# Kernel tuning notes

Measured on AMD Instinct MI355X. Metric: run time of the kernel, lower is better.

## Reference

```python
import jax, jax.numpy as jnp
import numpy as np

B, S, H = 4, 2048, 768
NUM_HEADS = 12
HEAD_DIM = H // NUM_HEADS


def setup_inputs() -> dict:
    key = jax.random.key(0)
    k1, k2, k3 = jax.random.split(key, 3)
    hidden_states = jax.random.normal(k1, (B, S, H), dtype=jnp.float32)
    # torch Linear weight [out,in]; store transposed [in,out] for x @ W
    w_qkv = jax.random.normal(k2, (H, 3 * H), dtype=jnp.float32) * (1.0 / np.sqrt(H))
    w_out = jax.random.normal(k3, (H, H), dtype=jnp.float32) * (1.0 / np.sqrt(H))
    return {"hidden_states": hidden_states, "w_qkv": w_qkv, "w_out": w_out}


def reference(hidden_states, w_qkv, w_out):
    b, s, h = hidden_states.shape
    qkv = hidden_states @ w_qkv                      # [b,s,3h]
    qkv = qkv.reshape(b, s, 3, NUM_HEADS, HEAD_DIM)
    qkv = jnp.transpose(qkv, (2, 0, 3, 1, 4))        # [3,b,nh,s,hd]
    q, k, v = qkv[0], qkv[1], qkv[2]
    scale = 1.0 / np.sqrt(HEAD_DIM).astype(np.float32)
    scores = jnp.einsum('bhqd,bhkd->bhqk', q, k) * scale   # [b,nh,s,s]
    causal = jnp.triu(jnp.ones((s, s), dtype=bool), k=1)
    scores = jnp.where(causal, jnp.float32(-jnp.inf), scores)
    attn = jax.nn.softmax(scores, axis=-1)
    # dropout is identity in eval mode
    out = jnp.einsum('bhqk,bhkd->bhqd', attn, v)      # [b,nh,s,hd]
    out = jnp.transpose(out, (0, 2, 1, 3)).reshape(b, s, h)
    return out @ w_out
```

## Files before the change

kernel.cpp:

```cpp
#include <hip/hip_runtime.h>
#include <stdint.h>

#define B_ 4
#define S_ 2048
#define H_ 768
#define NH_ 12
#define HD_ 64
#define BH_ (B_ * NH_)

#define QSCALE 0.18033688011112042f

typedef __attribute__((ext_vector_type(4))) float f32x4;
typedef __attribute__((ext_vector_type(16))) float f32x16;
typedef __attribute__((ext_vector_type(8))) __bf16 bf16x8;
typedef __attribute__((ext_vector_type(8))) unsigned short ushort8;
typedef __attribute__((ext_vector_type(2))) unsigned int u32x2;
typedef __attribute__((ext_vector_type(4))) unsigned int u32x4;

__device__ __forceinline__ unsigned short bf16rne(float f) {
  union { float f; unsigned int u; } v;
  v.f = f;
  unsigned int u = v.u;
  return (unsigned short)((u + 0x7fffu + ((u >> 16) & 1u)) >> 16);
}

#if __has_builtin(__builtin_amdgcn_cvt_pk_bf16_f32)
__device__ __forceinline__ unsigned int pk2(float a, float b) {
  auto r = __builtin_amdgcn_cvt_pk_bf16_f32(a, b);
  return *(unsigned int*)&r;
}
#else
__device__ __forceinline__ unsigned int pk2(float a, float b) {
  return (unsigned int)bf16rne(a) | ((unsigned int)bf16rne(b) << 16);
}
#endif

#if __has_builtin(__builtin_amdgcn_exp2f)
#define EXP2F(x) __builtin_amdgcn_exp2f(x)
#else
#define EXP2F(x) exp2f(x)
#endif

#if __has_builtin(__builtin_amdgcn_permlane32_swap)
__device__ __forceinline__ u32x2 permswap(unsigned a, unsigned b) {
  u32x2 r = __builtin_amdgcn_permlane32_swap(a, b, false, false);
  return r;
}
#else
__device__ __forceinline__ u32x2 permswap(unsigned a, unsigned b) {
  int l = (int)(threadIdx.x & 63);
  unsigned ap = (unsigned)__shfl((int)a, l ^ 32, 64);
  unsigned bp = (unsigned)__shfl((int)b, l ^ 32, 64);
  u32x2 r;
  r[0] = (l & 32) ? bp : a;
  r[1] = (l & 32) ? b : ap;
  return r;
}
#endif

__device__ __forceinline__ void gll16(const void* g, void* l) {
  __builtin_amdgcn_global_load_lds(
      (const __attribute__((address_space(1))) unsigned int*)g,
      (__attribute__((address_space(3))) unsigned int*)l, 16, 0, 0);
}

__device__ __forceinline__ void tconv_body(const float* __restrict__ in,
                                           unsigned short* __restrict__ out,
                                           int R, int C, int bx, int by,
                                           unsigned short (*tile)[72], int tid) {
  int c0 = bx * 64, r0 = by * 64;
#pragma unroll
  for (int i = 0; i < 4; ++i) {
    int c = i * 256 + tid;
    int row = c >> 4, col4 = (c & 15) * 4;
    float4 v = *(const float4*)(in + (size_t)(r0 + row) * C + c0 + col4);
    *(uint2*)(&tile[row][col4]) = (uint2){pk2(v.x, v.y), pk2(v.z, v.w)};
  }
  __syncthreads();
#pragma unroll
  for (int i = 0; i < 2; ++i) {
    int c = i * 256 + tid;
    int oc = c >> 3, r8 = (c & 7) * 8;
    ushort8 v;
#pragma unroll
    for (int j = 0; j < 8; ++j) v[j] = tile[r8 + j][oc];
    *(ushort8*)(out + (size_t)(c0 + oc) * R + r0 + r8) = v;
  }
}

__global__ __launch_bounds__(256) void prep_kernel(const float* __restrict__ hs,
                                                   const float* __restrict__ wqkv,
                                                   const float* __restrict__ wout,
                                                   unsigned short* __restrict__ Xbf,
                                                   unsigned short* __restrict__ Wqkvt,
                                                   unsigned short* __restrict__ Woutt) {
  __shared__ unsigned short tile[64][72];
  int bid = blockIdx.x, tid = threadIdx.x;
  if (bid < 3072) {
    int i = (bid * 256 + tid) * 8;
    const float4* p = (const float4*)(hs + i);
    float4 a = p[0], b = p[1];
    uint4 r = {pk2(a.x, a.y), pk2(a.z, a.w), pk2(b.x, b.y), pk2(b.z, b.w)};
    *(uint4*)(Xbf + i) = r;
  } else if (bid < 3504) {
    int idx = bid - 3072;
    tconv_body(wqkv, Wqkvt, 768, 2304, idx % 36, idx / 36, tile, tid);
  } else {
    int idx = bid - 3504;
    tconv_body(wout, Woutt, 768, 768, idx % 12, idx / 12, tile, tid);
  }
}

template <int MODE>
__device__ __forceinline__ void gemm_core(const unsigned short* __restrict__ A,
                                          const unsigned short* __restrict__ Bm,
                                          void* __restrict__ Cout, int N, int K,
                                          int bm, int bn,
                                          unsigned short* As, unsigned short* Bs) {
  int tid = threadIdx.x;
  int lane = tid & 63, wave = tid >> 6;
  int quad = lane >> 4, l16 = lane & 15;
  int wm = (wave & 1) * 64, wn = (wave >> 1) * 64;
  const unsigned short* Ag = A + (size_t)bm * 128 * K;
  const unsigned short* Bg = Bm + (size_t)bn * 128 * K;

  f32x4 zero = {0.f, 0.f, 0.f, 0.f};
  f32x4 acc[4][4];
#pragma unroll
  for (int mt = 0; mt < 4; ++mt)
#pragma unroll
    for (int nt = 0; nt < 4; ++nt) acc[mt][nt] = zero;

  for (int k0 = 0; k0 < K; k0 += 32) {
#pragma unroll
    for (int i = 0; i < 2; ++i) {
      int c = i * 256 + tid;
      int row = c >> 2, off = (c & 3) * 8;
      gll16(Ag + (size_t)row * K + k0 + off, As + c * 8);
      gll16(Bg + (size_t)row * K + k0 + off, Bs + c * 8);
    }
    __syncthreads();
    bf16x8 af[4], bf[4];
#pragma unroll
    for (int mt = 0; mt < 4; ++mt)
      af[mt] = *(const bf16x8*)(As + (wm + mt * 16 + l16) * 32 + quad * 8);
#pragma unroll
    for (int nt = 0; nt < 4; ++nt)
      bf[nt] = *(const bf16x8*)(Bs + (wn + nt * 16 + l16) * 32 + quad * 8);
#pragma unroll
    for (int mt = 0; mt < 4; ++mt)
#pragma unroll
      for (int nt = 0; nt < 4; ++nt) {
        if (MODE == 2)
          acc[mt][nt] = __builtin_amdgcn_mfma_f32_16x16x32_bf16(af[mt], bf[nt], acc[mt][nt], 0, 0, 0);
        else
          acc[mt][nt] = __builtin_amdgcn_mfma_f32_16x16x32_bf16(bf[nt], af[mt], acc[mt][nt], 0, 0, 0);
      }
    __syncthreads();
  }

  if (MODE == 0) {
    unsigned short* qkv = (unsigned short*)Cout;
    int which = (bn >= 6);
#pragma unroll
    for (int mt = 0; mt < 4; ++mt)
#pragma unroll
      for (int nt = 0; nt < 4; ++nt) {
        int f0 = bn * 128 + wn + nt * 16 + quad * 4;
        int tm = bm * 128 + wm + mt * 16 + l16;
        int rem = f0 - which * 768;
        int head = rem >> 6, d0 = rem & 63;
        int b = tm >> 11, s = tm & 2047;
        if (which == 0) {
          uint2 pkv = {pk2(acc[mt][nt][0] * QSCALE, acc[mt][nt][1] * QSCALE),
                       pk2(acc[mt][nt][2] * QSCALE, acc[mt][nt][3] * QSCALE)};
          *(uint2*)(qkv + (((size_t)b * NH_ + head) * S_ + s) * HD_ + d0) = pkv;
        } else {
          uint2 pkv = {pk2(acc[mt][nt][0], acc[mt][nt][1]),
                       pk2(acc[mt][nt][2], acc[mt][nt][3])};
          int t = s >> 6, kb = (s >> 5) & 1, row = s & 31;
          int dk = d0 >> 4, hh = (d0 >> 3) & 1, off = d0 & 7;
          *(uint2*)(qkv + ((size_t)(BH_ + b * NH_ + head)) * S_ * HD_ + t * 4096
                    + ((kb * 4 + dk) * 64 + hh * 32 + row) * 8 + off) = pkv;
        }
      }
  } else if (MODE == 2) {
    unsigned short* vt = (unsigned short*)Cout;
#pragma unroll
    for (int mt = 0; mt < 4; ++mt)
#pragma unroll
      for (int nt = 0; nt < 4; ++nt) {
        int f = bn * 128 + wn + nt * 16 + l16;
        int t0 = bm * 128 + wm + mt * 16 + quad * 4;
        int rem = f - 1536;
        int head = rem >> 6, d = rem & 63;
        int b = t0 >> 11, s0 = t0 & 2047;
        int tile = s0 >> 6, sin = s0 & 63;
        int ks = sin >> 4, hh = (sin >> 3) & 1, off = sin & 7;
        int db = d >> 5, drow = d & 31;
        uint2 pkv = {pk2(acc[mt][nt][0], acc[mt][nt][1]),
                     pk2(acc[mt][nt][2], acc[mt][nt][3])};
        *(uint2*)(vt + ((size_t)(b * NH_ + head)) * HD_ * S_ + tile * 4096
                  + ((db * 4 + ks) * 64 + hh * 32 + drow) * 8 + off) = pkv;
      }
  } else {
    float* outp = (float*)Cout;
#pragma unroll
    for (int mt = 0; mt < 4; ++mt)
#pragma unroll
      for (int nt = 0; nt < 4; ++nt) {
        int f0 = bn * 128 + wn + nt * 16 + quad * 4;
        int tm = bm * 128 + wm + mt * 16 + l16;
        *(f32x4*)(outp + (size_t)tm * N + f0) = acc[mt][nt];
      }
  }
}

__global__ __launch_bounds__(256) void gemm_qkv(const unsigned short* __restrict__ A,
                                                const unsigned short* __restrict__ Bm,
                                                unsigned short* __restrict__ QK,
                                                unsigned short* __restrict__ Vt) {
  __shared__ unsigned short As[128 * 32];
  __shared__ unsigned short Bs[128 * 32];
  int bm = blockIdx.x, bn = blockIdx.y;
  if (bn < 12)
    gemm_core<0>(A, Bm, QK, 2304, 768, bm, bn, As, Bs);
  else
    gemm_core<2>(A, Bm, Vt, 2304, 768, bm, bn, As, Bs);
}

__global__ __launch_bounds__(256) void gemm_out(const unsigned short* __restrict__ A,
                                                const unsigned short* __restrict__ Bm,
                                                float* __restrict__ Cout) {
  __shared__ unsigned short As[128 * 32];
  __shared__ unsigned short Bs[128 * 32];
  gemm_core<1>(A, Bm, Cout, 768, 768, blockIdx.x, blockIdx.y, As, Bs);
}

__global__ __launch_bounds__(256, 4) void attn_kernel(const unsigned short* __restrict__ Q,
                                                      const unsigned short* __restrict__ Kg,
                                                      const unsigned short* __restrict__ Vt,
                                                      unsigned short* __restrict__ O) {
  __shared__ unsigned short Ks[2][64 * 64];
  __shared__ unsigned short Vs[2][64 * 64];
  const int pi_[16] = {0, 1, 3, 5, 7, 9, 11, 13, 15, 14, 12, 10, 8, 6, 4, 2};
  int bh = blockIdx.x;
  int y = blockIdx.y;
  int qt = pi_[(bh + y) & 15];
  int tid = threadIdx.x, lane = tid & 63, wave = tid >> 6;
  int l32 = lane & 31, h = lane >> 5;
  const unsigned short* Qp = Q + (size_t)bh * S_ * HD_;
  int q0 = qt * 128;
  int qrow = q0 + wave * 32 + l32;
  int kmax_w = (q0 + wave * 32 + 31) >> 6;
  int kmax_b = 2 * qt + 1;

  const unsigned short* kS = Kg + (size_t)bh * S_ * HD_;
  const unsigned short* vS = Vt + (size_t)bh * HD_ * S_;

  auto stage = [&](int t, int buf) {
#pragma unroll
    for (int i = 0; i < 2; ++i) {
      int c = (i * 256 + tid) * 8;
      gll16(kS + (size_t)t * 4096 + c, &Ks[buf][c]);
      gll16(vS + (size_t)t * 4096 + c, &Vs[buf][c]);
    }
  };

  stage(0, 0);

  bf16x8 qf[4];
#pragma unroll
  for (int dk = 0; dk < 4; ++dk)
    qf[dk] = *(const bf16x8*)(Qp + (size_t)qrow * HD_ + dk * 16 + h * 8);

  bf16x8 ones;
#pragma unroll
  for (int j = 0; j < 8; ++j) ones[j] = (__bf16)1.0f;

  const int flin = lane * 8;

  f32x16 zero16;
#pragma unroll
  for (int j = 0; j < 16; ++j) zero16[j] = 0.f;
  f32x16 o[2], rsv;
  o[0] = zero16; o[1] = zero16; rsv = zero16;

  auto body = [&](int t, const unsigned short* Kb, const unsigned short* Vb) {
    f32x16 sf[2];
    sf[0] = zero16; sf[1] = zero16;
#pragma unroll
    for (int kb = 0; kb < 2; ++kb)
#pragma unroll
      for (int dk = 0; dk < 4; ++dk) {
        bf16x8 kf = *(const bf16x8*)(Kb + (kb * 4 + dk) * 512 + flin);
        sf[kb] = __builtin_amdgcn_mfma_f32_32x32x16_bf16(kf, qf[dk], sf[kb], 0, 0, 0);
      }

    if (t == kmax_w) {
#pragma unroll
      for (int kb = 0; kb < 2; ++kb)
#pragma unroll
        for (int r = 0; r < 16; ++r)
          if (t * 64 + kb * 32 + (r & 3) + 8 * (r >> 2) + 4 * h > qrow) sf[kb][r] = -1e30f;
    }

    unsigned p01[8], p23[8];
#pragma unroll
    for (int kb = 0; kb < 2; ++kb)
#pragma unroll
      for (int g = 0; g < 4; ++g) {
        p01[kb * 4 + g] = pk2(EXP2F(sf[kb][g * 4 + 0]), EXP2F(sf[kb][g * 4 + 1]));
        p23[kb * 4 + g] = pk2(EXP2F(sf[kb][g * 4 + 2]), EXP2F(sf[kb][g * 4 + 3]));
      }

#pragma unroll
    for (int ks = 0; ks < 4; ++ks) {
      u32x2 a02 = permswap(p01[2 * ks], p01[2 * ks + 1]);
      u32x2 a13 = permswap(p23[2 * ks], p23[2 * ks + 1]);
      u32x4 pu;
      pu[0] = a02[0]; pu[1] = a13[0]; pu[2] = a02[1]; pu[3] = a13[1];
      bf16x8 pf = *(bf16x8*)&pu;
      rsv = __builtin_amdgcn_mfma_f32_32x32x16_bf16(ones, pf, rsv, 0, 0, 0);
#pragma unroll
      for (int db = 0; db < 2; ++db) {
        bf16x8 vf = *(const bf16x8*)(Vb + (db * 4 + ks) * 512 + flin);
        o[db] = __builtin_amdgcn_mfma_f32_32x32x16_bf16(vf, pf, o[db], 0, 0, 0);
      }
    }
  };

  for (int t = 0; t <= kmax_b; t += 2) {
    __syncthreads();
    stage(t + 1, 1);
    if (t <= kmax_w) body(t, &Ks[0][0], &Vs[0][0]);
    __syncthreads();
    if (t + 2 <= kmax_b) stage(t + 2, 0);
    if (t + 1 <= kmax_w) body(t + 1, &Ks[1][0], &Vs[1][0]);
  }

  float inv = 1.f / rsv[0];
  int b = bh / NH_, hh = bh % NH_;
#pragma unroll
  for (int db = 0; db < 2; ++db)
#pragma unroll
    for (int g = 0; g < 4; ++g) {
      uint2 pkv = {pk2(o[db][g * 4 + 0] * inv, o[db][g * 4 + 1] * inv),
                   pk2(o[db][g * 4 + 2] * inv, o[db][g * 4 + 3] * inv)};
      int d0 = db * 32 + 8 * g + 4 * h;
      *(uint2*)(O + ((size_t)b * S_ + qrow) * H_ + hh * HD_ + d0) = pkv;
    }
}

extern "C" void kernel_launch(void* const* d_in, const int* in_sizes, int n_in,
                              void* d_out, int out_size, void* d_ws, size_t ws_size,
                              hipStream_t stream) {
  (void)in_sizes; (void)n_in; (void)out_size; (void)ws_size;
  const float* hs = (const float*)d_in[0];
  const float* wqkv = (const float*)d_in[1];
  const float* wout = (const float*)d_in[2];
  float* out = (float*)d_out;

  unsigned short* Xbf = (unsigned short*)d_ws;
  unsigned short* Wqkvt = Xbf + (size_t)8192 * 768;
  unsigned short* Woutt = Wqkvt + (size_t)2304 * 768;
  unsigned short* QK = Woutt + (size_t)768 * 768;
  unsigned short* Vt = QK + (size_t)2 * BH_ * S_ * HD_;
  unsigned short* Attn = Xbf;

  prep_kernel<<<3648, 256, 0, stream>>>(hs, wqkv, wout, Xbf, Wqkvt, Woutt);
  gemm_qkv<<<dim3(64, 18), 256, 0, stream>>>(Xbf, Wqkvt, QK, Vt);
  attn_kernel<<<dim3(48, 16), 256, 0, stream>>>(QK, QK + (size_t)BH_ * S_ * HD_, Vt, Attn);
  gemm_out<<<dim3(64, 6), 256, 0, stream>>>(Attn, Woutt, out);
}
```

Baseline: 198.2 us.

## Make attention kernel persistent with atomic work queue, longest tiles first

Replaces the static 48x16 attention grid with 1280 persistent blocks that pull (q-tile, head) jobs from a global atomic counter, with the longest causal tiles handed out first. The counter is reset inside the prep kernel. The aim is to balance the triangular causal workload across CUs and shorten the tail. In exchange it adds an atomic and two barriers per job, and it can lose the locality that the old permuted static order gave.

Result: slower. 212.0 us (+6.9%).

```diff
diff --git a/kernel.cpp b/kernel.cpp
--- a/kernel.cpp
+++ b/kernel.cpp
@@ -93,9 +93,11 @@
                                                    const float* __restrict__ wout,
                                                    unsigned short* __restrict__ Xbf,
                                                    unsigned short* __restrict__ Wqkvt,
-                                                   unsigned short* __restrict__ Woutt) {
+                                                   unsigned short* __restrict__ Woutt,
+                                                   unsigned int* __restrict__ ctr) {
   __shared__ unsigned short tile[64][72];
   int bid = blockIdx.x, tid = threadIdx.x;
+  if (bid == 0 && tid == 0) *ctr = 0u;
   if (bid < 3072) {
     int i = (bid * 256 + tid) * 8;
     const float4* p = (const float4*)(hs + i);
@@ -239,117 +241,125 @@
 
 __global__ __launch_bounds__(256, 4) void attn_kernel(const unsigned short* __restrict__ Q,
                                                       const unsigned short* __restrict__ Kg,
-                                                      const unsigned short* __restrict__ Vt,
-                                                      unsigned short* __restrict__ O) {
+                                                      const unsigned short* __restrict__ Vtg,
+                                                      unsigned short* __restrict__ O,
+                                                      unsigned int* __restrict__ ctr) {
   __shared__ unsigned short Ks[2][64 * 64];
   __shared__ unsigned short Vs[2][64 * 64];
-  const int pi_[16] = {0, 1, 3, 5, 7, 9, 11, 13, 15, 14, 12, 10, 8, 6, 4, 2};
-  int bh = blockIdx.x;
-  int y = blockIdx.y;
-  int qt = pi_[(bh + y) & 15];
+  __shared__ unsigned int jobS;
   int tid = threadIdx.x, lane = tid & 63, wave = tid >> 6;
   int l32 = lane & 31, h = lane >> 5;
-  const unsigned short* Qp = Q + (size_t)bh * S_ * HD_;
-  int q0 = qt * 128;
-  int qrow = q0 + wave * 32 + l32;
-  int kmax_w = (q0 + wave * 32 + 31) >> 6;
-  int kmax_b = 2 * qt + 1;
-
-  const unsigned short* kS = Kg + (size_t)bh * S_ * HD_;
-  const unsigned short* vS = Vt + (size_t)bh * HD_ * S_;
-
-  auto stage = [&](int t, int buf) {
-#pragma unroll
-    for (int i = 0; i < 2; ++i) {
-      int c = (i * 256 + tid) * 8;
-      gll16(kS + (size_t)t * 4096 + c, &Ks[buf][c]);
-      gll16(vS + (size_t)t * 4096 + c, &Vs[buf][c]);
+  const int flin = lane * 8;
+
+  bf16x8 ones;
+#pragma unroll
+  for (int j = 0; j < 8; ++j) ones[j] = (__bf16)1.0f;
+
+  f32x16 zero16;
+#pragma unroll
+  for (int j = 0; j < 16; ++j) zero16[j] = 0.f;
+
+  for (;;) {
+    __syncthreads();
+    if (tid == 0) jobS = atomicAdd(ctr, 1u);
+    __syncthreads();
+    unsigned j = jobS;
+    if (j >= 768u) break;
+    int qt = 15 - (int)(j / 48u);
+    int bh = (int)(j % 48u);
+
+    const unsigned short* Qp = Q + (size_t)bh * S_ * HD_;
+    const unsigned short* kS = Kg + (size_t)bh * S_ * HD_;
+    const unsigned short* vS = Vtg + (size_t)bh * HD_ * S_;
+    int q0 = qt * 128;
+    int qrow = q0 + wave * 32 + l32;
+    int kmax_w = (q0 + wave * 32 + 31) >> 6;
+    int kmax_b = 2 * qt + 1;
+
+    auto stage = [&](int t, int buf) {
+#pragma unroll
+      for (int i = 0; i < 2; ++i) {
+        int c = (i * 256 + tid) * 8;
+        gll16(kS + (size_t)t * 4096 + c, &Ks[buf][c]);
+        gll16(vS + (size_t)t * 4096 + c, &Vs[buf][c]);
+      }
+    };
+
+    stage(0, 0);
+
+    bf16x8 qf[4];
+#pragma unroll
+    for (int dk = 0; dk < 4; ++dk)
+      qf[dk] = *(const bf16x8*)(Qp + (size_t)qrow * HD_ + dk * 16 + h * 8);
+
+    f32x16 o[2], rsv;
+    o[0] = zero16; o[1] = zero16; rsv = zero16;
+
+    auto body = [&](int t, const unsigned short* Kb, const unsigned short* Vb) {
+      f32x16 sf[2];
+      sf[0] = zero16; sf[1] = zero16;
+#pragma unroll
+      for (int kb = 0; kb < 2; ++kb)
+#pragma unroll
+        for (int dk = 0; dk < 4; ++dk) {
+          bf16x8 kf = *(const bf16x8*)(Kb + (kb * 4 + dk) * 512 + flin);
+          sf[kb] = __builtin_amdgcn_mfma_f32_32x32x16_bf16(kf, qf[dk], sf[kb], 0, 0, 0);
+        }
+
+      if (t == kmax_w) {
+#pragma unroll
+        for (int kb = 0; kb < 2; ++kb)
+#pragma unroll
+          for (int r = 0; r < 16; ++r)
+            if (t * 64 + kb * 32 + (r & 3) + 8 * (r >> 2) + 4 * h > qrow) sf[kb][r] = -1e30f;
+      }
+
+      unsigned p01[8], p23[8];
+#pragma unroll
+      for (int kb = 0; kb < 2; ++kb)
+#pragma unroll
+        for (int g = 0; g < 4; ++g) {
+          p01[kb * 4 + g] = pk2(EXP2F(sf[kb][g * 4 + 0]), EXP2F(sf[kb][g * 4 + 1]));
+          p23[kb * 4 + g] = pk2(EXP2F(sf[kb][g * 4 + 2]), EXP2F(sf[kb][g * 4 + 3]));
+        }
+
+#pragma unroll
+      for (int ks = 0; ks < 4; ++ks) {
+        u32x2 a02 = permswap(p01[2 * ks], p01[2 * ks + 1]);
+        u32x2 a13 = permswap(p23[2 * ks], p23[2 * ks + 1]);
+        u32x4 pu;
+        pu[0] = a02[0]; pu[1] = a13[0]; pu[2] = a02[1]; pu[3] = a13[1];
+        bf16x8 pf = *(bf16x8*)&pu;
+        rsv = __builtin_amdgcn_mfma_f32_32x32x16_bf16(ones, pf, rsv, 0, 0, 0);
+#pragma unroll
+        for (int db = 0; db < 2; ++db) {
+          bf16x8 vf = *(const bf16x8*)(Vb + (db * 4 + ks) * 512 + flin);
+          o[db] = __builtin_amdgcn_mfma_f32_32x32x16_bf16(vf, pf, o[db], 0, 0, 0);
+        }
+      }
+    };
+
+    for (int t = 0; t <= kmax_b; t += 2) {
+      __syncthreads();
+      stage(t + 1, 1);
+      if (t <= kmax_w) body(t, &Ks[0][0], &Vs[0][0]);
+      __syncthreads();
+      if (t + 2 <= kmax_b) stage(t + 2, 0);
+      if (t + 1 <= kmax_w) body(t + 1, &Ks[1][0], &Vs[1][0]);
     }
-  };
-
-  stage(0, 0);
-
-  bf16x8 qf[4];
-#pragma unroll
-  for (int dk = 0; dk < 4; ++dk)
-    qf[dk] = *(const bf16x8*)(Qp + (size_t)qrow * HD_ + dk * 16 + h * 8);
-
-  bf16x8 ones;
-#pragma unroll
-  for (int j = 0; j < 8; ++j) ones[j] = (__bf16)1.0f;
-
-  const int flin = lane * 8;
-
-  f32x16 zero16;
-#pragma unroll
-  for (int j = 0; j < 16; ++j) zero16[j] = 0.f;
-  f32x16 o[2], rsv;
-  o[0] = zero16; o[1] = zero16; rsv = zero16;
-
-  auto body = [&](int t, const unsigned short* Kb, const unsigned short* Vb) {
-    f32x16 sf[2];
-    sf[0] = zero16; sf[1] = zero16;
-#pragma unroll
-    for (int kb = 0; kb < 2; ++kb)
-#pragma unroll
-      for (int dk = 0; dk < 4; ++dk) {
-        bf16x8 kf = *(const bf16x8*)(Kb + (kb * 4 + dk) * 512 + flin);
-        sf[kb] = __builtin_amdgcn_mfma_f32_32x32x16_bf16(kf, qf[dk], sf[kb], 0, 0, 0);
-      }
-
-    if (t == kmax_w) {
-#pragma unroll
-      for (int kb = 0; kb < 2; ++kb)
-#pragma unroll
-        for (int r = 0; r < 16; ++r)
-          if (t * 64 + kb * 32 + (r & 3) + 8 * (r >> 2) + 4 * h > qrow) sf[kb][r] = -1e30f;
-    }
-
-    unsigned p01[8], p23[8];
-#pragma unroll
-    for (int kb = 0; kb < 2; ++kb)
+
+    float inv = 1.f / rsv[0];
+    int b = bh / NH_, hh = bh % NH_;
+#pragma unroll
+    for (int db = 0; db < 2; ++db)
 #pragma unroll
       for (int g = 0; g < 4; ++g) {
-        p01[kb * 4 + g] = pk2(EXP2F(sf[kb][g * 4 + 0]), EXP2F(sf[kb][g * 4 + 1]));
-        p23[kb * 4 + g] = pk2(EXP2F(sf[kb][g * 4 + 2]), EXP2F(sf[kb][g * 4 + 3]));
-      }
-
-#pragma unroll
-    for (int ks = 0; ks < 4; ++ks) {
-      u32x2 a02 = permswap(p01[2 * ks], p01[2 * ks + 1]);
-      u32x2 a13 = permswap(p23[2 * ks], p23[2 * ks + 1]);
-      u32x4 pu;
-      pu[0] = a02[0]; pu[1] = a13[0]; pu[2] = a02[1]; pu[3] = a13[1];
-      bf16x8 pf = *(bf16x8*)&pu;
-      rsv = __builtin_amdgcn_mfma_f32_32x32x16_bf16(ones, pf, rsv, 0, 0, 0);
-#pragma unroll
-      for (int db = 0; db < 2; ++db) {
-        bf16x8 vf = *(const bf16x8*)(Vb + (db * 4 + ks) * 512 + flin);
-        o[db] = __builtin_amdgcn_mfma_f32_32x32x16_bf16(vf, pf, o[db], 0, 0, 0);
-      }
-    }
-  };
-
-  for (int t = 0; t <= kmax_b; t += 2) {
-    __syncthreads();
-    stage(t + 1, 1);
-    if (t <= kmax_w) body(t, &Ks[0][0], &Vs[0][0]);
-    __syncthreads();
-    if (t + 2 <= kmax_b) stage(t + 2, 0);
-    if (t + 1 <= kmax_w) body(t + 1, &Ks[1][0], &Vs[1][0]);
-  }
-
-  float inv = 1.f / rsv[0];
-  int b = bh / NH_, hh = bh % NH_;
-#pragma unroll
-  for (int db = 0; db < 2; ++db)
-#pragma unroll
-    for (int g = 0; g < 4; ++g) {
-      uint2 pkv = {pk2(o[db][g * 4 + 0] * inv, o[db][g * 4 + 1] * inv),
-                   pk2(o[db][g * 4 + 2] * inv, o[db][g * 4 + 3] * inv)};
-      int d0 = db * 32 + 8 * g + 4 * h;
-      *(uint2*)(O + ((size_t)b * S_ + qrow) * H_ + hh * HD_ + d0) = pkv;
-    }
+        uint2 pkv = {pk2(o[db][g * 4 + 0] * inv, o[db][g * 4 + 1] * inv),
+                     pk2(o[db][g * 4 + 2] * inv, o[db][g * 4 + 3] * inv)};
+        int d0 = db * 32 + 8 * g + 4 * h;
+        *(uint2*)(O + ((size_t)b * S_ + qrow) * H_ + hh * HD_ + d0) = pkv;
+      }
+  }
 }
 
 extern "C" void kernel_launch(void* const* d_in, const int* in_sizes, int n_in,
@@ -366,10 +376,11 @@
   unsigned short* Woutt = Wqkvt + (size_t)2304 * 768;
   unsigned short* QK = Woutt + (size_t)768 * 768;
   unsigned short* Vt = QK + (size_t)2 * BH_ * S_ * HD_;
+  unsigned int* ctr = (unsigned int*)(Vt + (size_t)BH_ * HD_ * S_);
   unsigned short* Attn = Xbf;
 
-  prep_kernel<<<3648, 256, 0, stream>>>(hs, wqkv, wout, Xbf, Wqkvt, Woutt);
+  prep_kernel<<<3648, 256, 0, stream>>>(hs, wqkv, wout, Xbf, Wqkvt, Woutt, ctr);
   gemm_qkv<<<dim3(64, 18), 256, 0, stream>>>(Xbf, Wqkvt, QK, Vt);
-  attn_kernel<<<dim3(48, 16), 256, 0, stream>>>(QK, QK + (size_t)BH_ * S_ * HD_, Vt, Attn);
+  attn_kernel<<<1280, 256, 0, stream>>>(QK, QK + (size_t)BH_ * S_ * HD_, Vt, Attn, ctr);
   gemm_out<<<dim3(64, 6), 256, 0, stream>>>(Attn, Woutt, out);
 }
```

## Use 64-row tiles for output GEMM and add MFMA priority hints in attention

Applied to the files above, without the earlier changes.

Replaces the output-projection GEMM, which used shared 128x128 tiles over 384 blocks, with a dedicated 64x128-tile kernel launched as 768 blocks so the 256 CUs are better filled. The attention kernel also wraps its MFMA sections in s_setprio to raise wave priority during matrix ops, aiming to overlap other waves' exp and softmax work. The new GEMM has no double buffering and lower per-block reuse. The priority hints may have little effect.

New measurement: 195.3 us. About the same (-1.5%).

```diff
diff --git a/kernel.cpp b/kernel.cpp
--- a/kernel.cpp
+++ b/kernel.cpp
@@ -184,7 +184,7 @@
                     + ((kb * 4 + dk) * 64 + hh * 32 + row) * 8 + off) = pkv;
         }
       }
-  } else if (MODE == 2) {
+  } else {
     unsigned short* vt = (unsigned short*)Cout;
 #pragma unroll
     for (int mt = 0; mt < 4; ++mt)
@@ -203,16 +203,6 @@
         *(uint2*)(vt + ((size_t)(b * NH_ + head)) * HD_ * S_ + tile * 4096
                   + ((db * 4 + ks) * 64 + hh * 32 + drow) * 8 + off) = pkv;
       }
-  } else {
-    float* outp = (float*)Cout;
-#pragma unroll
-    for (int mt = 0; mt < 4; ++mt)
-#pragma unroll
-      for (int nt = 0; nt < 4; ++nt) {
-        int f0 = bn * 128 + wn + nt * 16 + quad * 4;
-        int tm = bm * 128 + wm + mt * 16 + l16;
-        *(f32x4*)(outp + (size_t)tm * N + f0) = acc[mt][nt];
-      }
   }
 }
 
@@ -229,12 +219,61 @@
     gemm_core<2>(A, Bm, Vt, 2304, 768, bm, bn, As, Bs);
 }
 
-__global__ __launch_bounds__(256) void gemm_out(const unsigned short* __restrict__ A,
-                                                const unsigned short* __restrict__ Bm,
-                                                float* __restrict__ Cout) {
-  __shared__ unsigned short As[128 * 32];
+__global__ __launch_bounds__(256) void gemm_out64(const unsigned short* __restrict__ A,
+                                                  const unsigned short* __restrict__ Bm,
+                                                  float* __restrict__ Cout) {
+  __shared__ unsigned short As[64 * 32];
   __shared__ unsigned short Bs[128 * 32];
-  gemm_core<1>(A, Bm, Cout, 768, 768, blockIdx.x, blockIdx.y, As, Bs);
+  const int K = 768, N = 768;
+  int bm = blockIdx.x, bn = blockIdx.y;
+  int tid = threadIdx.x, lane = tid & 63, wave = tid >> 6;
+  int quad = lane >> 4, l16 = lane & 15;
+  int wn = wave * 32;
+  const unsigned short* Ag = A + (size_t)bm * 64 * K;
+  const unsigned short* Bg = Bm + (size_t)bn * 128 * K;
+
+  f32x4 zero = {0.f, 0.f, 0.f, 0.f};
+  f32x4 acc[4][2];
+#pragma unroll
+  for (int mt = 0; mt < 4; ++mt)
+#pragma unroll
+    for (int nt = 0; nt < 2; ++nt) acc[mt][nt] = zero;
+
+  for (int k0 = 0; k0 < K; k0 += 32) {
+    {
+      int row = tid >> 2, off = (tid & 3) * 8;
+      gll16(Ag + (size_t)row * K + k0 + off, As + tid * 8);
+    }
+#pragma unroll
+    for (int i = 0; i < 2; ++i) {
+      int c = i * 256 + tid;
+      int row = c >> 2, off = (c & 3) * 8;
+      gll16(Bg + (size_t)row * K + k0 + off, Bs + c * 8);
+    }
+    __syncthreads();
+    bf16x8 af[4], bf[2];
+#pragma unroll
+    for (int mt = 0; mt < 4; ++mt)
+      af[mt] = *(const bf16x8*)(As + (mt * 16 + l16) * 32 + quad * 8);
+#pragma unroll
+    for (int nt = 0; nt < 2; ++nt)
+      bf[nt] = *(const bf16x8*)(Bs + (wn + nt * 16 + l16) * 32 + quad * 8);
+#pragma unroll
+    for (int mt = 0; mt < 4; ++mt)
+#pragma unroll
+      for (int nt = 0; nt < 2; ++nt)
+        acc[mt][nt] = __builtin_amdgcn_mfma_f32_16x16x32_bf16(bf[nt], af[mt], acc[mt][nt], 0, 0, 0);
+    __syncthreads();
+  }
+
+#pragma unroll
+  for (int mt = 0; mt < 4; ++mt)
+#pragma unroll
+    for (int nt = 0; nt < 2; ++nt) {
+      int f0 = bn * 128 + wn + nt * 16 + quad * 4;
+      int tm = bm * 64 + mt * 16 + l16;
+      *(f32x4*)(Cout + (size_t)tm * N + f0) = acc[mt][nt];
+    }
 }
 
 __global__ __launch_bounds__(256, 4) void attn_kernel(const unsigned short* __restrict__ Q,
@@ -289,6 +328,7 @@
   auto body = [&](int t, const unsigned short* Kb, const unsigned short* Vb) {
     f32x16 sf[2];
     sf[0] = zero16; sf[1] = zero16;
+    __builtin_amdgcn_s_setprio(1);
 #pragma unroll
     for (int kb = 0; kb < 2; ++kb)
 #pragma unroll
@@ -296,6 +336,7 @@
         bf16x8 kf = *(const bf16x8*)(Kb + (kb * 4 + dk) * 512 + flin);
         sf[kb] = __builtin_amdgcn_mfma_f32_32x32x16_bf16(kf, qf[dk], sf[kb], 0, 0, 0);
       }
+    __builtin_amdgcn_s_setprio(0);
 
     if (t == kmax_w) {
 #pragma unroll
@@ -321,12 +362,14 @@
       u32x4 pu;
       pu[0] = a02[0]; pu[1] = a13[0]; pu[2] = a02[1]; pu[3] = a13[1];
       bf16x8 pf = *(bf16x8*)&pu;
+      __builtin_amdgcn_s_setprio(1);
       rsv = __builtin_amdgcn_mfma_f32_32x32x16_bf16(ones, pf, rsv, 0, 0, 0);
 #pragma unroll
       for (int db = 0; db < 2; ++db) {
         bf16x8 vf = *(const bf16x8*)(Vb + (db * 4 + ks) * 512 + flin);
         o[db] = __builtin_amdgcn_mfma_f32_32x32x16_bf16(vf, pf, o[db], 0, 0, 0);
       }
+      __builtin_amdgcn_s_setprio(0);
     }
   };
 
@@ -371,5 +414,5 @@
   prep_kernel<<<3648, 256, 0, stream>>>(hs, wqkv, wout, Xbf, Wqkvt, Woutt);
   gemm_qkv<<<dim3(64, 18), 256, 0, stream>>>(Xbf, Wqkvt, QK, Vt);
   attn_kernel<<<dim3(48, 16), 256, 0, stream>>>(QK, QK + (size_t)BH_ * S_ * HD_, Vt, Attn);
-  gemm_out<<<dim3(64, 6), 256, 0, stream>>>(Attn, Woutt, out);
-}
+  gemm_out64<<<dim3(128, 6), 256, 0, stream>>>(Attn, Woutt, out);
+}
```
